# Performance work log

Hardware: AMD Instinct MI355X
Metric: run time of the kernel (lower is better)

## Reference

```python
import jax, jax.numpy as jnp
import numpy as np

N_FEAT = 1024
N_LAYER = 4  # n_layer + 1 in the original module


def setup_inputs() -> dict:
    key = jax.random.key(0)
    kx, kw, kb = jax.random.split(key, 3)
    x = jax.random.normal(kx, (16384, N_FEAT), dtype=jnp.float32)
    weight_w = jax.random.normal(kw, (N_LAYER, N_FEAT), dtype=jnp.float32)
    weight_b = jax.random.normal(kb, (N_LAYER, N_FEAT), dtype=jnp.float32)
    return {"x": x, "weight_w": weight_w, "weight_b": weight_b}


def reference(x, weight_w, weight_b):
    # Original per layer: x_{i+1} = x0 @ x_i^T @ w_i + b_i + x_i  (per sample).
    # (x0 x_i^T) w = x0 * <x_i, w>, so we use the O(n) equivalent form and
    # never materialize the [B, n, n] outer product.
    x0 = x  # [B, n]
    xi = x0
    for i in range(N_LAYER):
        xiw = jnp.einsum("bn,n->b", xi, weight_w[i])  # [B]
        xi = x0 * xiw[:, None] + weight_b[i][None, :] + xi
    return xi
```

## Files before the change

kernel.cpp:

```cpp
#include <hip/hip_runtime.h>

#define N_FEAT 1024
#define N_LAYER 4

__global__ __launch_bounds__(256) void crossnet_kernel(
    const float* __restrict__ x,
    const float* __restrict__ weight_w,
    const float* __restrict__ weight_b,
    float* __restrict__ out,
    int n_rows) {
  const int wave = threadIdx.x >> 6;
  const int lane = threadIdx.x & 63;
  const int row = blockIdx.x * 4 + wave;
  if (row >= n_rows) return;

  const float4* xrow = (const float4*)(x + (size_t)row * N_FEAT);
  float4* orow = (float4*)(out + (size_t)row * N_FEAT);

  float4 x0[4], xi[4];
#pragma unroll
  for (int c = 0; c < 4; ++c) {
    x0[c] = xrow[c * 64 + lane];
    xi[c] = x0[c];
  }

#pragma unroll
  for (int l = 0; l < N_LAYER; ++l) {
    const float4* wrow = (const float4*)(weight_w + l * N_FEAT);
    const float4* brow = (const float4*)(weight_b + l * N_FEAT);

    float partial = 0.0f;
#pragma unroll
    for (int c = 0; c < 4; ++c) {
      float4 w = wrow[c * 64 + lane];
      partial += xi[c].x * w.x;
      partial += xi[c].y * w.y;
      partial += xi[c].z * w.z;
      partial += xi[c].w * w.w;
    }
#pragma unroll
    for (int off = 32; off > 0; off >>= 1)
      partial += __shfl_xor(partial, off, 64);

#pragma unroll
    for (int c = 0; c < 4; ++c) {
      float4 b = brow[c * 64 + lane];
      xi[c].x = fmaf(x0[c].x, partial, b.x + xi[c].x);
      xi[c].y = fmaf(x0[c].y, partial, b.y + xi[c].y);
      xi[c].z = fmaf(x0[c].z, partial, b.z + xi[c].z);
      xi[c].w = fmaf(x0[c].w, partial, b.w + xi[c].w);
    }
  }

#pragma unroll
  for (int c = 0; c < 4; ++c)
    orow[c * 64 + lane] = xi[c];
}

extern "C" void kernel_launch(void* const* d_in, const int* in_sizes, int n_in,
                              void* d_out, int out_size, void* d_ws, size_t ws_size,
                              hipStream_t stream) {
  const float* x = (const float*)d_in[0];
  const float* ww = (const float*)d_in[1];
  const float* wb = (const float*)d_in[2];
  float* out = (float*)d_out;

  int n_rows = in_sizes[0] / N_FEAT;
  int n_blocks = (n_rows + 3) / 4;
  crossnet_kernel<<<n_blocks, 256, 0, stream>>>(x, ww, wb, out, n_rows);
}
```

Before: 124.7 us.

## Collapse layer recurrence into scalar coefficient with batched wave reductions

Rewrites the recurrence algebraically: x_i = A_i*x0 + cumsum(b), so each row needs the dot products of x0 with every w_i plus dot products of the cumulative bias with w_i. All reductions are computed in a single pass and share one shuffle loop, replacing four sequential reduce-then-update stages. This removes the serial dependency between layers and the per-layer vector updates. In exchange it recomputes bias-weight dot products per row and changes floating-point summation order.

```diff
diff --git a/kernel.cpp b/kernel.cpp
--- a/kernel.cpp
+++ b/kernel.cpp
@@ -17,44 +17,63 @@
   const float4* xrow = (const float4*)(x + (size_t)row * N_FEAT);
   float4* orow = (float4*)(out + (size_t)row * N_FEAT);
 
-  float4 x0[4], xi[4];
+  float4 x0[4];
+  float4 csum[4];
+  float p[N_LAYER] = {0.f, 0.f, 0.f, 0.f};
+  float e[N_LAYER] = {0.f, 0.f, 0.f, 0.f};
+
 #pragma unroll
   for (int c = 0; c < 4; ++c) {
     x0[c] = xrow[c * 64 + lane];
-    xi[c] = x0[c];
+
+    float4 w[N_LAYER];
+#pragma unroll
+    for (int i = 0; i < N_LAYER; ++i)
+      w[i] = ((const float4*)(weight_w + i * N_FEAT))[c * 64 + lane];
+
+#pragma unroll
+    for (int i = 0; i < N_LAYER; ++i) {
+      p[i] += x0[c].x * w[i].x + x0[c].y * w[i].y +
+              x0[c].z * w[i].z + x0[c].w * w[i].w;
+    }
+
+    float4 cum = make_float4(0.f, 0.f, 0.f, 0.f);
+#pragma unroll
+    for (int i = 0; i < N_LAYER; ++i) {
+      if (i > 0) {
+        e[i] += cum.x * w[i].x + cum.y * w[i].y +
+                cum.z * w[i].z + cum.w * w[i].w;
+      }
+      float4 b = ((const float4*)(weight_b + i * N_FEAT))[c * 64 + lane];
+      cum.x += b.x; cum.y += b.y; cum.z += b.z; cum.w += b.w;
+    }
+    csum[c] = cum;
   }
 
 #pragma unroll
-  for (int l = 0; l < N_LAYER; ++l) {
-    const float4* wrow = (const float4*)(weight_w + l * N_FEAT);
-    const float4* brow = (const float4*)(weight_b + l * N_FEAT);
+  for (int off = 32; off > 0; off >>= 1) {
+#pragma unroll
+    for (int i = 0; i < N_LAYER; ++i) p[i] += __shfl_xor(p[i], off, 64);
+#pragma unroll
+    for (int i = 1; i < N_LAYER; ++i) e[i] += __shfl_xor(e[i], off, 64);
+  }
 
-    float partial = 0.0f;
+  float A = 1.f;
 #pragma unroll
-    for (int c = 0; c < 4; ++c) {
-      float4 w = wrow[c * 64 + lane];
-      partial += xi[c].x * w.x;
-      partial += xi[c].y * w.y;
-      partial += xi[c].z * w.z;
-      partial += xi[c].w * w.w;
-    }
-#pragma unroll
-    for (int off = 32; off > 0; off >>= 1)
-      partial += __shfl_xor(partial, off, 64);
-
-#pragma unroll
-    for (int c = 0; c < 4; ++c) {
-      float4 b = brow[c * 64 + lane];
-      xi[c].x = fmaf(x0[c].x, partial, b.x + xi[c].x);
-      xi[c].y = fmaf(x0[c].y, partial, b.y + xi[c].y);
-      xi[c].z = fmaf(x0[c].z, partial, b.z + xi[c].z);
-      xi[c].w = fmaf(x0[c].w, partial, b.w + xi[c].w);
-    }
+  for (int i = 0; i < N_LAYER; ++i) {
+    float s = A * p[i] + e[i];
+    A += s;
   }
 
 #pragma unroll
-  for (int c = 0; c < 4; ++c)
-    orow[c * 64 + lane] = xi[c];
+  for (int c = 0; c < 4; ++c) {
+    float4 o;
+    o.x = fmaf(x0[c].x, A, csum[c].x);
+    o.y = fmaf(x0[c].y, A, csum[c].y);
+    o.z = fmaf(x0[c].z, A, csum[c].z);
+    o.w = fmaf(x0[c].w, A, csum[c].w);
+    orow[c * 64 + lane] = o;
+  }
 }
 
 extern "C" void kernel_launch(void* const* d_in, const int* in_sizes, int n_in,
```

After: 125.7 us. No clear change (+0.8%).
